# Optimization experiments

Hardware: AMD Instinct MI355X
Metric: run time of the kernel (lower is better)

## Reference

```python
import jax, jax.numpy as jnp
import numpy as np

N_NODES = 100000
N_EDGES = 6400000
PENALTY_N = 0.1  # init arg `n`


def setup_inputs() -> dict:
    key = jax.random.key(0)
    k1, k2, k3, k4, k5 = jax.random.split(key, 5)
    edge_index = jax.random.randint(k1, (2, N_EDGES), 0, N_NODES, dtype=jnp.int64 if jax.config.read('jax_enable_x64') else jnp.int32)
    edge_weight = jax.random.uniform(k2, (N_EDGES,), dtype=jnp.float32)
    nodes_yield_rate = jax.random.uniform(k3, (N_NODES,), dtype=jnp.float32)
    nodes_traffic = jax.random.uniform(k4, (N_NODES,), dtype=jnp.float32)
    nodes_cost = jax.random.uniform(k5, (N_NODES,), dtype=jnp.float32)
    return {
        'edge_index': edge_index,
        'edge_weight': edge_weight,
        'nodes_yield_rate': nodes_yield_rate,
        'nodes_traffic': nodes_traffic,
        'nodes_cost': nodes_cost,
    }


def reference(edge_index, edge_weight, nodes_yield_rate, nodes_traffic, nodes_cost):
    # Original loop reads src/dst traffic from the ORIGINAL tensor and accumulates
    # updates into a clone; both branches are equivalent to:
    #   src -= |diff| * n * w ; dst += |diff| * n * w
    # i.e. a pure per-edge scatter-add with no edge-order dependency.
    src = edge_index[0]
    dst = edge_index[1]
    diff = nodes_traffic[src] - nodes_traffic[dst]          # [E]
    transfer = jnp.abs(diff) * PENALTY_N * edge_weight      # [E]
    new_traffic = nodes_traffic.at[src].add(-transfer).at[dst].add(transfer)
    total_service_efficiency = jnp.sum(nodes_yield_rate * new_traffic - nodes_cost)
    return new_traffic, total_service_efficiency
```

## Files before the change

### kernel.cpp

```cpp
#include <hip/hip_runtime.h>

#define PENALTY_N 0.1f
#define NPART 4
#define CP 25000
#define MAX_BPP 64
#define ABLK 1024

__global__ __launch_bounds__(ABLK) void part_scatter_kernel(
    const int* __restrict__ src_idx,
    const int* __restrict__ dst_idx,
    const float* __restrict__ w,
    const float* __restrict__ traffic,
    float* __restrict__ scratch,
    float* __restrict__ out_scalar,
    int nE, int nN, int Bpp) {
    __shared__ float hist[CP];

    const int p = blockIdx.x / Bpp;
    const int b = blockIdx.x % Bpp;
    const int lo = p * CP;
    const unsigned csz = (unsigned)min(CP, nN - lo);
    const int tid = threadIdx.x;

    if (blockIdx.x == 0 && tid == 0) *out_scalar = 0.0f;

    for (int i = tid; i < CP; i += ABLK) hist[i] = 0.0f;
    __syncthreads();

    const int nvec = nE >> 2;
    const int4* __restrict__ src4 = (const int4*)src_idx;
    const int4* __restrict__ dst4 = (const int4*)dst_idx;
    const float4* __restrict__ w4 = (const float4*)w;
    const int stride = Bpp * ABLK;

    for (int v = b * ABLK + tid; v < nvec; v += stride) {
        int4 s = src4[v];
        int4 d = dst4[v];
        float4 ww = w4[v];

        #pragma unroll
        for (int k = 0; k < 4; ++k) {
            int si = (&s.x)[k];
            int di = (&d.x)[k];
            unsigned so = (unsigned)(si - lo);
            unsigned doo = (unsigned)(di - lo);
            bool inS = so < csz;
            bool inD = doo < csz;
            if (inS || inD) {
                float t = fabsf(traffic[si] - traffic[di]) * (PENALTY_N * (&ww.x)[k]);
                if (inS) atomicAdd(&hist[so], -t);
                if (inD) atomicAdd(&hist[doo], t);
            }
        }
    }
    for (int e = (nvec << 2) + b * ABLK + tid; e < nE; e += stride) {
        int si = src_idx[e];
        int di = dst_idx[e];
        unsigned so = (unsigned)(si - lo);
        unsigned doo = (unsigned)(di - lo);
        bool inS = so < csz;
        bool inD = doo < csz;
        if (inS || inD) {
            float t = fabsf(traffic[si] - traffic[di]) * (PENALTY_N * w[e]);
            if (inS) atomicAdd(&hist[so], -t);
            if (inD) atomicAdd(&hist[doo], t);
        }
    }

    __syncthreads();
    float* dst = scratch + (size_t)blockIdx.x * CP;
    for (unsigned i = tid; i < csz; i += ABLK) dst[i] = hist[i];
}

__global__ __launch_bounds__(256) void part_reduce_kernel(
    const float* __restrict__ scratch,
    const float* __restrict__ traffic,
    const float* __restrict__ yield_rate,
    const float* __restrict__ cost,
    float* __restrict__ out,
    int nN, int Bpp) {
    const int tid = blockIdx.x * blockDim.x + threadIdx.x;
    const int stride = gridDim.x * blockDim.x;

    float acc = 0.0f;
    for (int i = tid; i < nN; i += stride) {
        int p = i / CP;
        int off = i - p * CP;
        const float* base = scratch + (size_t)p * Bpp * CP + off;
        float s = traffic[i];
        for (int b = 0; b < Bpp; ++b) s += base[(size_t)b * CP];
        out[i] = s;
        acc = fmaf(yield_rate[i], s, acc) - cost[i];
    }

    #pragma unroll
    for (int off = 32; off > 0; off >>= 1) acc += __shfl_down(acc, off, 64);

    __shared__ float wsum[4];
    const int lane = threadIdx.x & 63;
    const int wid = threadIdx.x >> 6;
    if (lane == 0) wsum[wid] = acc;
    __syncthreads();
    if (threadIdx.x == 0)
        atomicAdd(&out[nN], wsum[0] + wsum[1] + wsum[2] + wsum[3]);
}

__global__ void init_out_kernel(const float* __restrict__ traffic,
                                float* __restrict__ out, int nN) {
    int i = blockIdx.x * blockDim.x + threadIdx.x;
    if (i < nN) out[i] = traffic[i];
    else if (i == nN) out[i] = 0.0f;
}

__global__ __launch_bounds__(256) void edge_scatter_kernel(
    const int* __restrict__ src_idx, const int* __restrict__ dst_idx,
    const float* __restrict__ w, const float* __restrict__ traffic,
    float* __restrict__ out, int nE) {
    const int tid = blockIdx.x * blockDim.x + threadIdx.x;
    const int stride = gridDim.x * blockDim.x;
    for (int e = tid; e < nE; e += stride) {
        int s = src_idx[e];
        int d = dst_idx[e];
        float t = fabsf(traffic[s] - traffic[d]) * (PENALTY_N * w[e]);
        atomicAdd(&out[s], -t);
        atomicAdd(&out[d], t);
    }
}

__global__ __launch_bounds__(256) void reduce_kernel(
    const float* __restrict__ new_traffic, const float* __restrict__ yield_rate,
    const float* __restrict__ cost, float* __restrict__ total, int nN) {
    const int tid = blockIdx.x * blockDim.x + threadIdx.x;
    const int stride = gridDim.x * blockDim.x;
    float acc = 0.0f;
    for (int i = tid; i < nN; i += stride)
        acc = fmaf(yield_rate[i], new_traffic[i], acc) - cost[i];
    #pragma unroll
    for (int off = 32; off > 0; off >>= 1) acc += __shfl_down(acc, off, 64);
    __shared__ float wsum[4];
    const int lane = threadIdx.x & 63;
    const int wid = threadIdx.x >> 6;
    if (lane == 0) wsum[wid] = acc;
    __syncthreads();
    if (threadIdx.x == 0)
        atomicAdd(total, wsum[0] + wsum[1] + wsum[2] + wsum[3]);
}

extern "C" void kernel_launch(void* const* d_in, const int* in_sizes, int n_in,
                              void* d_out, int out_size, void* d_ws, size_t ws_size,
                              hipStream_t stream) {
    const int* edge_index = (const int*)d_in[0];
    const float* edge_weight = (const float*)d_in[1];
    const float* nodes_yield = (const float*)d_in[2];
    const float* nodes_traffic = (const float*)d_in[3];
    const float* nodes_cost = (const float*)d_in[4];
    float* out = (float*)d_out;

    const int nE = in_sizes[1];
    const int nN = in_sizes[2];
    const int* src_idx = edge_index;
    const int* dst_idx = edge_index + nE;

    const int P = (nN + CP - 1) / CP;
    int Bpp = (int)(ws_size / ((size_t)P * CP * sizeof(float)));
    if (Bpp > MAX_BPP) Bpp = MAX_BPP;

    if (Bpp >= 4 && P <= 8) {
        float* scratch = (float*)d_ws;
        part_scatter_kernel<<<P * Bpp, ABLK, 0, stream>>>(
            src_idx, dst_idx, edge_weight, nodes_traffic,
            scratch, out + nN, nE, nN, Bpp);
        part_reduce_kernel<<<256, 256, 0, stream>>>(
            scratch, nodes_traffic, nodes_yield, nodes_cost, out, nN, Bpp);
    } else {
        int grid = (nN + 1 + 255) / 256;
        init_out_kernel<<<grid, 256, 0, stream>>>(nodes_traffic, out, nN);
        edge_scatter_kernel<<<2048, 256, 0, stream>>>(src_idx, dst_idx,
                                                      edge_weight, nodes_traffic,
                                                      out, nE);
        reduce_kernel<<<256, 256, 0, stream>>>(out, nodes_yield, nodes_cost,
                                               out + nN, nN);
    }
}
```

Baseline: 227.0 us.

## Shrink node partitions, raise blocks per partition, unroll partial-sum reduction

Node partition size drops from 25000 to 20000, so there are five partitions instead of four. The cap on blocks per partition rises from 64 to 102, and the scatter kernel's launch bounds request more resident blocks per CU, which is possible now that the LDS histogram is smaller. The reduce kernel now sums partial histograms with an 8-way unrolled loop into four independent accumulators and launches enough blocks to cover every node, aiming for more memory-level parallelism. The cost is that each edge is scanned once per partition, so more partitions mean more redundant edge reads, and more blocks mean more scratch to reduce.

New measurement: 229.3 us. Within noise of the previous version (+1.0%).

```diff
diff --git a/kernel.cpp b/kernel.cpp
--- a/kernel.cpp
+++ b/kernel.cpp
@@ -1,12 +1,11 @@
 #include <hip/hip_runtime.h>
 
 #define PENALTY_N 0.1f
-#define NPART 4
-#define CP 25000
-#define MAX_BPP 64
+#define CP 20000
+#define MAX_BPP 102
 #define ABLK 1024
 
-__global__ __launch_bounds__(ABLK) void part_scatter_kernel(
+__global__ __launch_bounds__(ABLK, 8) void part_scatter_kernel(
     const int* __restrict__ src_idx,
     const int* __restrict__ dst_idx,
     const float* __restrict__ w,
@@ -69,7 +68,7 @@
 
     __syncthreads();
     float* dst = scratch + (size_t)blockIdx.x * CP;
-    for (unsigned i = tid; i < csz; i += ABLK) dst[i] = hist[i];
+    for (int i = tid; i < CP; i += ABLK) dst[i] = hist[i];
 }
 
 __global__ __launch_bounds__(256) void part_reduce_kernel(
@@ -86,9 +85,27 @@
     for (int i = tid; i < nN; i += stride) {
         int p = i / CP;
         int off = i - p * CP;
-        const float* base = scratch + (size_t)p * Bpp * CP + off;
-        float s = traffic[i];
-        for (int b = 0; b < Bpp; ++b) s += base[(size_t)b * CP];
+        const float* base = scratch + ((size_t)p * Bpp + 0) * CP + off;
+
+        float s0 = traffic[i], s1 = 0.0f, s2 = 0.0f, s3 = 0.0f;
+        int b = 0;
+        for (; b + 8 <= Bpp; b += 8) {
+            const float* q = base + (size_t)b * CP;
+            float a0 = q[0 * (size_t)CP];
+            float a1 = q[1 * (size_t)CP];
+            float a2 = q[2 * (size_t)CP];
+            float a3 = q[3 * (size_t)CP];
+            float a4 = q[4 * (size_t)CP];
+            float a5 = q[5 * (size_t)CP];
+            float a6 = q[6 * (size_t)CP];
+            float a7 = q[7 * (size_t)CP];
+            s0 += a0 + a4;
+            s1 += a1 + a5;
+            s2 += a2 + a6;
+            s3 += a3 + a7;
+        }
+        for (; b < Bpp; ++b) s0 += base[(size_t)b * CP];
+        float s = (s0 + s1) + (s2 + s3);
         out[i] = s;
         acc = fmaf(yield_rate[i], s, acc) - cost[i];
     }
@@ -170,7 +187,8 @@
         part_scatter_kernel<<<P * Bpp, ABLK, 0, stream>>>(
             src_idx, dst_idx, edge_weight, nodes_traffic,
             scratch, out + nN, nE, nN, Bpp);
-        part_reduce_kernel<<<256, 256, 0, stream>>>(
+        int rgrid = (nN + 255) / 256;
+        part_reduce_kernel<<<rgrid, 256, 0, stream>>>(
             scratch, nodes_traffic, nodes_yield, nodes_cost, out, nN, Bpp);
     } else {
         int grid = (nN + 1 + 255) / 256;
```
